# Performance work log

Hardware: AMD Instinct MI355X
Metric: run time of the kernel (lower is better)

## Reference

```python
import jax, jax.numpy as jnp
import numpy as np

NUM_FREQUENCIES = 128
NUM_TIMES = 128
SIGMA = 0.1
BATCH = 32
LENGTH = 8192


def setup_inputs() -> dict:
    key = jax.random.key(0)
    signal = jax.random.normal(key, (BATCH, LENGTH), dtype=jnp.float32)
    return {"signal": signal}


def reference(signal) -> jnp.ndarray:
    # signal: [B, L]
    B, L = signal.shape
    # Matches torch.linspace(...).long(): linspace then truncate toward zero.
    time_centers = jnp.linspace(0.0, L - 1, NUM_TIMES).astype(jnp.int32).astype(jnp.float32)  # [T]
    freq_vals = jnp.linspace(0.0, L // 2, NUM_FREQUENCIES).astype(jnp.int32).astype(jnp.float32)  # [F]
    t = jnp.arange(L, dtype=jnp.float32)  # [L]
    sigma_w = SIGMA * L
    # Gaussian windows, one per time center: [T, L]
    window = jnp.exp(-0.5 * ((t[None, :] - time_centers[:, None]) / sigma_w) ** 2)
    # Real part of exp(-2j*pi*f*l/L) modulation: [F, L]
    two_pi = jnp.float32(2.0 * np.pi)
    cos_mod = jnp.cos(two_pi * freq_vals[:, None] * t[None, :] / L)
    # Original loop stores a complex dot product into a real tensor -> real part only:
    # result[b, f, t] = sum_l signal[b,l] * window[t,l] * cos(2*pi*f*l/L)
    windowed = jnp.einsum('bl,tl->btl', signal, window)  # [B, T, L]
    result = jnp.einsum('btl,fl->bft', windowed, cos_mod)  # [B, F, T]
    return result
```

## Files before the change

### kernel.cpp

```cpp
#include <hip/hip_runtime.h>
#include <hip/hip_bf16.h>
#include <math.h>


#define L_ 8192
#define B_ 32
#define SPLITK 16
#define KCHUNK 512
#define BK 64
#define STEPS 8

typedef _Float16 half8 __attribute__((ext_vector_type(8)));
typedef __fp16 fp16x2 __attribute__((ext_vector_type(2)));
typedef float float4v __attribute__((ext_vector_type(4)));

#define H_ 0.001220703125f
#define H64_ 0.078125f
#define QQ_ 0.99999850988388061523f
#define CSTEP_ 7.66990393942594528198e-4f


__global__ __launch_bounds__(256, 3) void gabor_gemm_kernel(
    const float* __restrict__ signal, float* __restrict__ partial) {
  const int bx = blockIdx.x;
  const int fhalf = bx & 1;
  const int thalf = (bx >> 1) & 1;
  const int bgrp = (bx >> 2) & 7;
  const int kc = bx >> 5;
  const int tid = threadIdx.x;

  __shared__ _Float16 As[2][64 * 64];
  __shared__ _Float16 Bs[2][64][72];
  __shared__ _Float16 Sg[2][4][64];

  const int lane = tid & 63;
  const int wv = tid >> 6;
  const int wmt = (wv >> 1) * 32;
  const int wnf = (wv & 1) * 32;
  const int frow = lane & 15;
  const int quad = lane >> 4;

  const int r0 = tid >> 3;
  const int c8 = (tid & 7) * 8;
  const int cidx = tid & 7;

  const float tstep = 8191.0f / 127.0f;
  const float fstep = 4096.0f / 127.0f;
  const int l0f = kc * KCHUNK;

  float x[2];
  int m[2];
  int dfv[2];
  float dlt[2];
  float k2[2];
#pragma unroll
  for (int rep = 0; rep < 2; ++rep) {
    const int row = r0 + rep * 32;
    const float tc = truncf((float)(thalf * 64 + row) * tstep);
    const int fv = (int)((float)(fhalf * 64 + row) * fstep);
    x[rep] = ((float)(l0f + c8) - tc) * H_;
    m[rep] = __mul24(fv, l0f + c8) & (L_ - 1);
    dfv[rep] = fv << 6;
    dlt[rep] = (float)fv * CSTEP_;
    k2[rep] = 2.0f * __cosf(dlt[rep]);
  }

  float4v acc[4][2][2];
#pragma unroll
  for (int bi = 0; bi < 4; ++bi)
#pragma unroll
    for (int i = 0; i < 2; ++i)
#pragma unroll
      for (int j = 0; j < 2; ++j) acc[bi][i][j] = (float4v)(0.0f);

  const float* sigbase = signal + (size_t)(bgrp * 4) * L_;

  union H8 {
    fp16x2 h2[4];
    half8 h8;
  };

#define STAGE(s, buf)                                                        \
  {                                                                          \
    const int l0 = l0f + (s)*BK;                                             \
    Sg[buf][wv][lane] = (_Float16)sigbase[(size_t)wv * L_ + l0 + lane];      \
    _Pragma("unroll") for (int rep = 0; rep < 2; ++rep) {                    \
      const int row = r0 + rep * 32;                                         \
                              \
      float w0 = __expf(-0.5f * x[rep] * x[rep]);                            \
      float ratio = __expf(-H_ * (x[rep] + 0.5f * H_));                      \
                              \
      const float a = (float)m[rep] * CSTEP_;                                \
      float cm2 = __cosf(a);                                                 \
      float cm1 = __cosf(a + dlt[rep]);                                      \
      H8 hw, hb;                                                             \
      float wp = w0;                                                         \
      float wn = w0 * ratio;                                                 \
      ratio *= QQ_;                                                          \
      hw.h2[0] = __builtin_amdgcn_cvt_pkrtz(wp, wn);                         \
      hb.h2[0] = __builtin_amdgcn_cvt_pkrtz(cm2, cm1);                       \
      _Pragma("unroll") for (int p = 1; p < 4; ++p) {                        \
        wp = wn * ratio;                                                     \
        ratio *= QQ_;                                                        \
        wn = wp * ratio;                                                     \
        ratio *= QQ_;                                                        \
        hw.h2[p] = __builtin_amdgcn_cvt_pkrtz(wp, wn);                       \
        const float c0 = __builtin_fmaf(k2[rep], cm1, -cm2);                 \
        const float c1 = __builtin_fmaf(k2[rep], c0, -cm1);                  \
        hb.h2[p] = __builtin_amdgcn_cvt_pkrtz(c0, c1);                       \
        cm2 = c0;                                                            \
        cm1 = c1;                                                            \
      }                                                                      \
      *(half8*)&As[buf][(row << 6) + ((cidx ^ (row & 7)) << 3)] = hw.h8;     \
      *(half8*)&Bs[buf][row][c8] = hb.h8;                                    \
      x[rep] += H64_;                                                        \
      m[rep] = (m[rep] + dfv[rep]) & (L_ - 1);                               \
    }                                                                        \
  }

  STAGE(0, 0);

  for (int s = 0; s < STEPS; ++s) {
    const int cb = s & 1, nb = cb ^ 1;
    __syncthreads();
#pragma unroll
    for (int kh = 0; kh < 2; ++kh) {
      const int kk = kh * 32 + quad * 8;
      const int chunk = kh * 4 + quad;
      half8 aw[2], bf[2];
#pragma unroll
      for (int i = 0; i < 2; ++i) {
        const int r = wmt + i * 16 + frow;
        aw[i] = *(const half8*)&As[cb][(r << 6) + ((chunk ^ (r & 7)) << 3)];
      }
#pragma unroll
      for (int j = 0; j < 2; ++j)
        bf[j] = *(const half8*)&Bs[cb][wnf + j * 16 + frow][kk];
#pragma unroll
      for (int bi = 0; bi < 4; ++bi) {
        const half8 sgv = *(const half8*)&Sg[cb][bi][kk];
        const half8 a0 = aw[0] * sgv;
        const half8 a1 = aw[1] * sgv;
        acc[bi][0][0] = __builtin_amdgcn_mfma_f32_16x16x32_f16(a0, bf[0],
                                                               acc[bi][0][0], 0, 0, 0);
        acc[bi][0][1] = __builtin_amdgcn_mfma_f32_16x16x32_f16(a0, bf[1],
                                                               acc[bi][0][1], 0, 0, 0);
        acc[bi][1][0] = __builtin_amdgcn_mfma_f32_16x16x32_f16(a1, bf[0],
                                                               acc[bi][1][0], 0, 0, 0);
        acc[bi][1][1] = __builtin_amdgcn_mfma_f32_16x16x32_f16(a1, bf[1],
                                                               acc[bi][1][1], 0, 0, 0);
      }
    }
    if (s + 1 < STEPS) STAGE(s + 1, nb);
  }

  const int tq = quad * 4;
#pragma unroll
  for (int bi = 0; bi < 4; ++bi) {
    float* pbase = partial + ((size_t)(kc * B_ + bgrp * 4 + bi) << 14);
#pragma unroll
    for (int i = 0; i < 2; ++i) {
      const int t = thalf * 64 + wmt + i * 16 + tq;
#pragma unroll
      for (int j = 0; j < 2; ++j) {
        const int f = fhalf * 64 + wnf + j * 16 + frow;
        *(float4v*)(pbase + f * 128 + t) = acc[bi][i][j];
      }
    }
  }
}

__global__ __launch_bounds__(256) void gabor_reduce_kernel(
    const float* __restrict__ partial, float* __restrict__ out) {
  const size_t gi = ((size_t)blockIdx.x * 256 + threadIdx.x) * 4;
  float4v s = (float4v)(0.0f);
#pragma unroll
  for (int kc = 0; kc < SPLITK; ++kc)
    s += *(const float4v*)(partial + (size_t)kc * 524288 + gi);
  *(float4v*)(out + gi) = s;
}

extern "C" void kernel_launch(void* const* d_in, const int* in_sizes, int n_in,
                              void* d_out, int out_size, void* d_ws, size_t ws_size,
                              hipStream_t stream) {
  const float* signal = (const float*)d_in[0];
  float* out = (float*)d_out;
  float* partial = (float*)d_ws;
  gabor_gemm_kernel<<<dim3(512), dim3(256), 0, stream>>>(signal, partial);
  gabor_reduce_kernel<<<dim3(512), dim3(256), 0, stream>>>(partial, out);
}
```

Before: 82.02 us.

## Split frequency tile into quarters, double grid, preload signal chunk once

Each block now covers 64 time centers by 32 frequencies instead of 64 by 64, so the GEMM grid doubles to 1024 blocks. Occupancy in launch bounds rises from 3 to 4 blocks, and each thread holds half as many accumulators. The signal chunk for the whole K range is converted to fp16 once into shared memory at kernel start rather than staged every step. The cost is that the Gaussian window tile is recomputed by twice as many blocks, and each block issues fewer MFMAs per window element it generates.

```diff
diff --git a/kernel.cpp b/kernel.cpp
--- a/kernel.cpp
+++ b/kernel.cpp
@@ -20,23 +20,23 @@
 #define CSTEP_ 7.66990393942594528198e-4f
 
 
-__global__ __launch_bounds__(256, 3) void gabor_gemm_kernel(
+__global__ __launch_bounds__(256, 4) void gabor_gemm_kernel(
     const float* __restrict__ signal, float* __restrict__ partial) {
   const int bx = blockIdx.x;
-  const int fhalf = bx & 1;
-  const int thalf = (bx >> 1) & 1;
-  const int bgrp = (bx >> 2) & 7;
-  const int kc = bx >> 5;
+  const int fq = bx & 3;
+  const int tq64 = (bx >> 2) & 1;
+  const int bgrp = (bx >> 3) & 7;
+  const int kc = bx >> 6;
   const int tid = threadIdx.x;
 
   __shared__ _Float16 As[2][64 * 64];
-  __shared__ _Float16 Bs[2][64][72];
-  __shared__ _Float16 Sg[2][4][64];
+  __shared__ _Float16 Bs[2][32][72];
+  __shared__ _Float16 Sg[4][KCHUNK];
 
   const int lane = tid & 63;
   const int wv = tid >> 6;
-  const int wmt = (wv >> 1) * 32;
-  const int wnf = (wv & 1) * 32;
+  const int wmt = (wv & 1) * 32;
+  const int wnf = (wv >> 1) * 16;
   const int frow = lane & 15;
   const int quad = lane >> 4;
 
@@ -48,73 +48,77 @@
   const float fstep = 4096.0f / 127.0f;
   const int l0f = kc * KCHUNK;
 
+  {
+    const int bi = tid >> 6;
+    const int e8 = (tid & 63) * 8;
+    const float* sp = signal + (size_t)(bgrp * 4 + bi) * L_ + l0f + e8;
+    union { fp16x2 h2[4]; half8 h8; } sh;
+#pragma unroll
+    for (int p = 0; p < 4; ++p)
+      sh.h2[p] = __builtin_amdgcn_cvt_pkrtz(sp[2 * p], sp[2 * p + 1]);
+    *(half8*)&Sg[bi][e8] = sh.h8;
+  }
+
   float x[2];
-  int m[2];
-  int dfv[2];
-  float dlt[2];
-  float k2[2];
+  int m, dfv;
+  float dlt, k2;
 #pragma unroll
   for (int rep = 0; rep < 2; ++rep) {
-    const int row = r0 + rep * 32;
-    const float tc = truncf((float)(thalf * 64 + row) * tstep);
-    const int fv = (int)((float)(fhalf * 64 + row) * fstep);
+    const float tc = truncf((float)(tq64 * 64 + r0 + rep * 32) * tstep);
     x[rep] = ((float)(l0f + c8) - tc) * H_;
-    m[rep] = __mul24(fv, l0f + c8) & (L_ - 1);
-    dfv[rep] = fv << 6;
-    dlt[rep] = (float)fv * CSTEP_;
-    k2[rep] = 2.0f * __cosf(dlt[rep]);
+  }
+  {
+    const int fv = (int)((float)(fq * 32 + r0) * fstep);
+    m = __mul24(fv, l0f + c8) & (L_ - 1);
+    dfv = fv << 6;
+    dlt = (float)fv * CSTEP_;
+    k2 = 2.0f * __cosf(dlt);
   }
 
-  float4v acc[4][2][2];
+  float4v acc[4][2];
 #pragma unroll
   for (int bi = 0; bi < 4; ++bi)
 #pragma unroll
-    for (int i = 0; i < 2; ++i)
-#pragma unroll
-      for (int j = 0; j < 2; ++j) acc[bi][i][j] = (float4v)(0.0f);
+    for (int i = 0; i < 2; ++i) acc[bi][i] = (float4v)(0.0f);
 
-  const float* sigbase = signal + (size_t)(bgrp * 4) * L_;
-
-  union H8 {
-    fp16x2 h2[4];
-    half8 h8;
-  };
+  union H8 { fp16x2 h2[4]; half8 h8; };
 
 #define STAGE(s, buf)                                                        \
   {                                                                          \
-    const int l0 = l0f + (s)*BK;                                             \
-    Sg[buf][wv][lane] = (_Float16)sigbase[(size_t)wv * L_ + l0 + lane];      \
     _Pragma("unroll") for (int rep = 0; rep < 2; ++rep) {                    \
       const int row = r0 + rep * 32;                                         \
-                              \
       float w0 = __expf(-0.5f * x[rep] * x[rep]);                            \
       float ratio = __expf(-H_ * (x[rep] + 0.5f * H_));                      \
-                              \
-      const float a = (float)m[rep] * CSTEP_;                                \
-      float cm2 = __cosf(a);                                                 \
-      float cm1 = __cosf(a + dlt[rep]);                                      \
-      H8 hw, hb;                                                             \
+      H8 hw;                                                                 \
       float wp = w0;                                                         \
       float wn = w0 * ratio;                                                 \
       ratio *= QQ_;                                                          \
       hw.h2[0] = __builtin_amdgcn_cvt_pkrtz(wp, wn);                         \
-      hb.h2[0] = __builtin_amdgcn_cvt_pkrtz(cm2, cm1);                       \
       _Pragma("unroll") for (int p = 1; p < 4; ++p) {                        \
         wp = wn * ratio;                                                     \
         ratio *= QQ_;                                                        \
         wn = wp * ratio;                                                     \
         ratio *= QQ_;                                                        \
         hw.h2[p] = __builtin_amdgcn_cvt_pkrtz(wp, wn);                       \
-        const float c0 = __builtin_fmaf(k2[rep], cm1, -cm2);                 \
-        const float c1 = __builtin_fmaf(k2[rep], c0, -cm1);                  \
+      }                                                                      \
+      *(half8*)&As[buf][(row << 6) + ((cidx ^ (row & 7)) << 3)] = hw.h8;     \
+      x[rep] += H64_;                                                        \
+    }                                                                        \
+    {                                                                        \
+      const float a = (float)m * CSTEP_;                                     \
+      float cm2 = __cosf(a);                                                 \
+      float cm1 = __cosf(a + dlt);                                           \
+      H8 hb;                                                                 \
+      hb.h2[0] = __builtin_amdgcn_cvt_pkrtz(cm2, cm1);                       \
+      _Pragma("unroll") for (int p = 1; p < 4; ++p) {                        \
+        const float c0 = __builtin_fmaf(k2, cm1, -cm2);                      \
+        const float c1 = __builtin_fmaf(k2, c0, -cm1);                       \
         hb.h2[p] = __builtin_amdgcn_cvt_pkrtz(c0, c1);                       \
         cm2 = c0;                                                            \
         cm1 = c1;                                                            \
       }                                                                      \
-      *(half8*)&As[buf][(row << 6) + ((cidx ^ (row & 7)) << 3)] = hw.h8;     \
-      *(half8*)&Bs[buf][row][c8] = hb.h8;                                    \
-      x[rep] += H64_;                                                        \
-      m[rep] = (m[rep] + dfv[rep]) & (L_ - 1);                               \
+      *(half8*)&Bs[buf][r0][c8] = hb.h8;                                     \
+      m = (m + dfv) & (L_ - 1);                                              \
     }                                                                        \
   }
 
@@ -127,45 +131,36 @@
     for (int kh = 0; kh < 2; ++kh) {
       const int kk = kh * 32 + quad * 8;
       const int chunk = kh * 4 + quad;
-      half8 aw[2], bf[2];
+      half8 aw[2], bf;
 #pragma unroll
       for (int i = 0; i < 2; ++i) {
         const int r = wmt + i * 16 + frow;
         aw[i] = *(const half8*)&As[cb][(r << 6) + ((chunk ^ (r & 7)) << 3)];
       }
-#pragma unroll
-      for (int j = 0; j < 2; ++j)
-        bf[j] = *(const half8*)&Bs[cb][wnf + j * 16 + frow][kk];
+      bf = *(const half8*)&Bs[cb][wnf + frow][kk];
 #pragma unroll
       for (int bi = 0; bi < 4; ++bi) {
-        const half8 sgv = *(const half8*)&Sg[cb][bi][kk];
+        const half8 sgv = *(const half8*)&Sg[bi][s * BK + kk];
         const half8 a0 = aw[0] * sgv;
         const half8 a1 = aw[1] * sgv;
-        acc[bi][0][0] = __builtin_amdgcn_mfma_f32_16x16x32_f16(a0, bf[0],
-                                                               acc[bi][0][0], 0, 0, 0);
-        acc[bi][0][1] = __builtin_amdgcn_mfma_f32_16x16x32_f16(a0, bf[1],
-                                                               acc[bi][0][1], 0, 0, 0);
-        acc[bi][1][0] = __builtin_amdgcn_mfma_f32_16x16x32_f16(a1, bf[0],
-                                                               acc[bi][1][0], 0, 0, 0);
-        acc[bi][1][1] = __builtin_amdgcn_mfma_f32_16x16x32_f16(a1, bf[1],
-                                                               acc[bi][1][1], 0, 0, 0);
+        acc[bi][0] = __builtin_amdgcn_mfma_f32_16x16x32_f16(a0, bf,
+                                                            acc[bi][0], 0, 0, 0);
+        acc[bi][1] = __builtin_amdgcn_mfma_f32_16x16x32_f16(a1, bf,
+                                                            acc[bi][1], 0, 0, 0);
       }
     }
     if (s + 1 < STEPS) STAGE(s + 1, nb);
   }
 
-  const int tq = quad * 4;
+  const int tqr = quad * 4;
 #pragma unroll
   for (int bi = 0; bi < 4; ++bi) {
     float* pbase = partial + ((size_t)(kc * B_ + bgrp * 4 + bi) << 14);
+    const int f = fq * 32 + wnf + frow;
 #pragma unroll
     for (int i = 0; i < 2; ++i) {
-      const int t = thalf * 64 + wmt + i * 16 + tq;
-#pragma unroll
-      for (int j = 0; j < 2; ++j) {
-        const int f = fhalf * 64 + wnf + j * 16 + frow;
-        *(float4v*)(pbase + f * 128 + t) = acc[bi][i][j];
-      }
+      const int t = tq64 * 64 + wmt + i * 16 + tqr;
+      *(float4v*)(pbase + f * 128 + t) = acc[bi][i];
     }
   }
 }
@@ -186,6 +181,6 @@
   const float* signal = (const float*)d_in[0];
   float* out = (float*)d_out;
   float* partial = (float*)d_ws;
-  gabor_gemm_kernel<<<dim3(512), dim3(256), 0, stream>>>(signal, partial);
+  gabor_gemm_kernel<<<dim3(1024), dim3(256), 0, stream>>>(signal, partial);
   gabor_reduce_kernel<<<dim3(512), dim3(256), 0, stream>>>(partial, out);
 }
```

Measured after the change: 81.29 us. No clear change (-0.9%).
